# Optimization experiments

Hardware: AMD Instinct MI355X
Metric: run time of the kernel (lower is better)

## Reference

```python
import jax, jax.numpy as jnp
import numpy as np

SQRT_QKV_DIM = 8.0  # sqrt(qkv_dim=64)


def setup_inputs() -> dict:
    key = jax.random.key(0)
    ks = jax.random.split(key, 8)
    B, H, T, M, d, hid = 4, 16, 512, 512, 64, 16
    return {
        "q": jax.random.normal(ks[0], (B, H, T, d), dtype=jnp.float32),
        "k": jax.random.normal(ks[1], (B, H, M, d), dtype=jnp.float32),
        "v": jax.random.normal(ks[2], (B, H, M, d), dtype=jnp.float32),
        "D_TM": jax.random.uniform(ks[3], (B, T, M), dtype=jnp.float32),
        "mix1_weight": jax.random.uniform(ks[4], (H, 2, hid), minval=-0.7071, maxval=0.7071, dtype=jnp.float32),
        "mix1_bias": jax.random.uniform(ks[5], (H, hid), minval=-0.7071, maxval=0.7071, dtype=jnp.float32),
        "mix2_weight": jax.random.uniform(ks[6], (H, hid, 1), minval=-0.25, maxval=0.25, dtype=jnp.float32),
        "mix2_bias": jax.random.uniform(ks[7], (H, 1), minval=-0.25, maxval=0.25, dtype=jnp.float32),
    }


def reference(q, k, v, D_TM, mix1_weight, mix1_bias, mix2_weight, mix2_bias):
    B, H, T, d = q.shape
    Mc = k.shape[2]
    # scaled dot-product score: (B,H,T,M)
    dot_score = jnp.einsum("bhtd,bhmd->bhtm", q, k) / SQRT_QKV_DIM
    # per-head 2->hidden->1 MLP mixing dot score and distance bias.
    # Avoid explicit stack: linear layer over the 2 score channels expands as
    # dot*W1[:,0,:] + D*W1[:,1,:].  ms1: (B,H,T,M,hid)
    w1_dot = mix1_weight[:, 0, :][None, :, None, None, :]   # (1,H,1,1,hid)
    w1_dist = mix1_weight[:, 1, :][None, :, None, None, :]
    ms1 = (dot_score[..., None] * w1_dot
           + D_TM[:, None, :, :, None] * w1_dist
           + mix1_bias[None, :, None, None, :])
    ms1 = jax.nn.relu(ms1)
    # hidden -> 1: mixed_scores (B,H,T,M)
    mixed = jnp.einsum("bhtmc,hc->bhtm", ms1, mix2_weight[:, :, 0])
    mixed = mixed + mix2_bias[:, 0][None, :, None, None]
    weights = jax.nn.softmax(mixed, axis=3)
    out = jnp.einsum("bhtm,bhmd->bhtd", weights, v)   # (B,H,T,d)
    return out.transpose(0, 2, 1, 3).reshape(B, T, H * d)
```

## Files before the change

kernel.cpp:

```cpp
#include <hip/hip_runtime.h>
#include <stdint.h>

typedef __attribute__((ext_vector_type(8))) short short8;
typedef __attribute__((ext_vector_type(4))) float floatx4;
typedef __attribute__((ext_vector_type(2))) float float2v;

#define MFMA(a, b, c) __builtin_amdgcn_mfma_f32_16x16x32_bf16(a, b, c, 0, 0, 0)

union Frag { uint32_t u[4]; short8 s; };

__device__ __forceinline__ void packsplit(float a, float b, uint32_t& hi, uint32_t& lo) {
    uint32_t ua = __float_as_uint(a), ub = __float_as_uint(b);
    uint32_t ha = ua & 0xFFFF0000u, hb = ub & 0xFFFF0000u;
    float ra = a - __uint_as_float(ha);
    float rb = b - __uint_as_float(hb);
    hi = __builtin_amdgcn_perm(ub, ua, 0x07060302u);
    lo = __builtin_amdgcn_perm(__float_as_uint(rb), __float_as_uint(ra), 0x07060302u);
}

__device__ __forceinline__ float fexp2(float x) {
#if __has_builtin(__builtin_amdgcn_exp2f)
    return __builtin_amdgcn_exp2f(x);
#else
    return exp2f(x);
#endif
}

__device__ __forceinline__ void bar_lds() {
    asm volatile("s_waitcnt lgkmcnt(0)" ::: "memory");
    __builtin_amdgcn_s_barrier();
    __builtin_amdgcn_sched_barrier(0);
}


__global__ __launch_bounds__(512)
void msmha_flash(const float* __restrict__ qg, const float* __restrict__ kg,
                 const float* __restrict__ vg, const float* __restrict__ Dg,
                 const float* __restrict__ m1w, const float* __restrict__ m1b,
                 const float* __restrict__ m2w, const float* __restrict__ m2b,
                 float* __restrict__ outg) {
    __shared__ __align__(16) uint32_t sm[17408];
    __shared__ __align__(16) float4 wlds[16];

    const int tid   = threadIdx.x;
    const int w     = tid >> 6;
    const int group = w >> 2;
    const int gw    = w & 3;
    const int lane  = tid & 63;
    const int col   = lane & 15;
    const int quad  = lane >> 4;
    const int gtid  = tid & 255;

    const int bid = blockIdx.x;
    const int wgT = bid >> 6;
    const int bh  = bid & 63;
    const int h   = bh & 15;
    const int b   = bh >> 4;
    const int t0g = wgT * 64;

    const size_t base = (size_t)bh * 512 * 64;
    const float LOG2E = 1.4426950408889634f;

    if (tid < 16) {
        const float w1d = m1w[h * 32 + tid];
        const float w1s = m1w[h * 32 + 16 + tid];
        const float b1  = m1b[h * 16 + tid];
        const float w2  = m2w[h * 16 + tid];
        wlds[tid] = make_float4(w1d * (0.125f * LOG2E), w1s * LOG2E, b1 * LOG2E, 0.5f * w2);
    }

    const int krow = 16 * gw + (lane >> 2);
    const int kqt  = lane & 3;
    const int ksw  = (krow & 7) << 2;
    const int rsw  = (col & 7) << 2;
    const int dgrp = gtid & 15;
    const int m4   = gtid >> 4;
    const int cpV  = (2 * m4 + 8 * ((dgrp >> 1) & 3)) & 31;
    const int rsel = col >> 3;

    const int gb = group * 8704;
    uint32_t* KH = sm + gb;
    uint32_t* KL = sm + gb + 2048;
    uint32_t* VH = sm + gb + 4096;
    uint32_t* VL = sm + gb + 6400;

    const int moff = group * 256;
    const float* kc = kg + base + (size_t)moff * 64;
    const float* vc = vg + base + (size_t)moff * 64;
    const float* Dc = Dg + ((size_t)b * 512 + t0g + gw * 16 + col) * 512 + moff + quad * 4;

    float4 kp[4];
#pragma unroll
    for (int i = 0; i < 4; ++i)
        kp[i] = *(const float4*)(kc + (size_t)krow * 64 + 16 * i + 4 * kqt);

    float sA = 0.f, sB = 0.f, sC = 0.f;
#pragma unroll 1
    for (int c = 0; c < 16; ++c) {
        const float w2 = m2w[h * 16 + c];
        sA = fmaf(w2, m1w[h * 32 + c], sA);
        sB = fmaf(w2, m1w[h * 32 + 16 + c], sB);
        sC = fmaf(w2, m1b[h * 16 + c], sC);
    }
    const float Ac = sA * (0.0625f * LOG2E);
    const float Bc = sB * (0.5f * LOG2E);
    const float Cc = fmaf(0.5f, sC, m2b[h]) * LOG2E;

    Frag qh[2], ql[2];
    {
        const float* qrow = qg + base + (size_t)(t0g + gw * 16 + col) * 64;
#pragma unroll
        for (int ks = 0; ks < 2; ++ks) {
            const float4 f0 = *(const float4*)(qrow + ks * 32 + quad * 8);
            const float4 f1 = *(const float4*)(qrow + ks * 32 + quad * 8 + 4);
            packsplit(f0.x, f0.y, qh[ks].u[0], ql[ks].u[0]);
            packsplit(f0.z, f0.w, qh[ks].u[1], ql[ks].u[1]);
            packsplit(f1.x, f1.y, qh[ks].u[2], ql[ks].u[2]);
            packsplit(f1.z, f1.w, qh[ks].u[3], ql[ks].u[3]);
        }
    }

    float lsx = 0.f, lsy = 0.f;
    floatx4 oacc[4];
#pragma unroll
    for (int dt = 0; dt < 4; ++dt) oacc[dt] = floatx4{0.f, 0.f, 0.f, 0.f};

    const float2v Ac2 = {Ac, Ac}, Bc2 = {Bc, Bc}, Cc2 = {Cc, Cc};

#pragma unroll
    for (int mc = 0; mc < 4; ++mc) {
        float4 vp[4], dp[4];
#pragma unroll
        for (int i = 0; i < 4; ++i)
            vp[i] = *(const float4*)(vc + (size_t)(mc * 64 + 4 * m4 + i) * 64 + dgrp * 4);
#pragma unroll
        for (int mt = 0; mt < 4; ++mt)
            dp[mt] = *(const float4*)(Dc + mc * 64 + mt * 16);

#pragma unroll
        for (int i = 0; i < 4; ++i) {
            uint32_t h0, l0, h1, l1;
            packsplit(kp[i].x, kp[i].y, h0, l0);
            packsplit(kp[i].z, kp[i].w, h1, l1);
            const int off = (8 * i + 2 * kqt) ^ ksw;
            *(uint2*)(KH + krow * 32 + off) = make_uint2(h0, h1);
            *(uint2*)(KL + krow * 32 + off) = make_uint2(l0, l1);
        }
        if (mc < 3) {
#pragma unroll
            for (int i = 0; i < 4; ++i)
                kp[i] = *(const float4*)(kc + (size_t)((mc + 1) * 64 + krow) * 64 + 16 * i + 4 * kqt);
        }
        bar_lds();

        floatx4 sc[4];
        __builtin_amdgcn_s_setprio(1);
#pragma unroll
        for (int mt = 0; mt < 4; ++mt) {
            floatx4 acc = {0.f, 0.f, 0.f, 0.f};
#pragma unroll
            for (int ks = 0; ks < 2; ++ks) {
                const int ro = (mt * 16 + col) * 32 + ((16 * ks + 4 * quad) ^ rsw);
                Frag ah, al;
                ah.s = *(const short8*)(KH + ro);
                al.s = *(const short8*)(KL + ro);
                acc = MFMA(ah.s, qh[ks].s, acc);
                acc = MFMA(ah.s, ql[ks].s, acc);
                acc = MFMA(al.s, qh[ks].s, acc);
            }
            sc[mt] = acc;
        }
        __builtin_amdgcn_s_setprio(0);

#pragma unroll
        for (int jj = 0; jj < 4; ++jj) {
            uint32_t h0, l0, h1, l1;
            packsplit(((const float*)&vp[0])[jj], ((const float*)&vp[1])[jj], h0, l0);
            packsplit(((const float*)&vp[2])[jj], ((const float*)&vp[3])[jj], h1, l1);
            const int d = 4 * dgrp + jj;
            *(uint2*)(VH + d * 36 + cpV) = make_uint2(h0, h1);
            *(uint2*)(VL + d * 36 + cpV) = make_uint2(l0, l1);
        }

        float2v scp[8], dvp[8], mixp[8];
#pragma unroll
        for (int mt = 0; mt < 4; ++mt) {
            scp[2 * mt]     = float2v{sc[mt][0], sc[mt][1]};
            scp[2 * mt + 1] = float2v{sc[mt][2], sc[mt][3]};
            dvp[2 * mt]     = float2v{dp[mt].x, dp[mt].y};
            dvp[2 * mt + 1] = float2v{dp[mt].z, dp[mt].w};
        }
#pragma unroll
        for (int e = 0; e < 8; ++e) mixp[e] = dvp[e] * Bc2 + Cc2;
#pragma unroll 4
        for (int c = 0; c < 16; ++c) {
            const float4 wv = wlds[c];
            const float2v wx = {wv.x, wv.x}, wy = {wv.y, wv.y};
            const float2v wz = {wv.z, wv.z}, ww = {wv.w, wv.w};
#pragma unroll
            for (int e = 0; e < 8; ++e) {
                const float2v hh = scp[e] * wx + (dvp[e] * wy + wz);
                const float2v ah = __builtin_elementwise_max(hh, -hh);
                mixp[e] = ah * ww + mixp[e];
            }
        }
#pragma unroll
        for (int e = 0; e < 8; ++e) {
            const float2v s2 = scp[e] * Ac2 + mixp[e];
            const float px = fexp2(s2.x);
            const float py = fexp2(s2.y);
            scp[e] = float2v{px, py};
            lsx += px; lsy += py;
        }

        bar_lds();

        const int prow = (gw * 16 + col) * 32;
#pragma unroll
        for (int mt = 0; mt < 4; ++mt) {
            uint32_t h0, l0, h1, l1;
            packsplit(scp[2 * mt].x, scp[2 * mt].y, h0, l0);
            packsplit(scp[2 * mt + 1].x, scp[2 * mt + 1].y, h1, l1);
            const int off = (mt * 8 + 2 * quad) ^ rsw;
            *(uint2*)(KH + prow + off) = make_uint2(h0, h1);
            *(uint2*)(KL + prow + off) = make_uint2(l0, l1);
        }

        __builtin_amdgcn_s_setprio(1);
#pragma unroll
        for (int ks = 0; ks < 2; ++ks) {
            const int po = prow + ((16 * ks + 4 * quad) ^ rsw);
            Frag pah, pal;
            pah.s = *(const short8*)(KH + po);
            pal.s = *(const short8*)(KL + po);
#pragma unroll
            for (int dt = 0; dt < 4; ++dt) {
                const int cbd = ((16 * ks + 4 * quad) + 8 * ((2 * dt + rsel) & 3)) & 31;
                const int vo = (dt * 16 + col) * 36 + cbd;
                Frag bhv, blv;
                bhv.s = *(const short8*)(VH + vo);
                blv.s = *(const short8*)(VL + vo);
                oacc[dt] = MFMA(pah.s, bhv.s, oacc[dt]);
                oacc[dt] = MFMA(pah.s, blv.s, oacc[dt]);
                oacc[dt] = MFMA(pal.s, bhv.s, oacc[dt]);
            }
        }
        __builtin_amdgcn_s_setprio(0);
    }

    bar_lds();

    float lsum = lsx + lsy;
    lsum += __shfl_xor(lsum, 16, 64);
    lsum += __shfl_xor(lsum, 32, 64);

    float* smf = (float*)sm;
    if (group == 1) {
        if (quad == 0) smf[12864 + gw * 16 + col] = lsum;
        const int t = gw * 16 + quad * 4;
#pragma unroll
        for (int dt = 0; dt < 4; ++dt)
#pragma unroll
            for (int r = 0; r < 4; ++r)
                smf[8704 + (t + r) * 65 + dt * 16 + col] = oacc[dt][r];
    }
    bar_lds();
    if (group == 0) {
        const float l1c = smf[12864 + gw * 16 + col];
        const float rdn = 1.f / (lsum + l1c);
        float rdT[4];
#pragma unroll
        for (int r = 0; r < 4; ++r)
            rdT[r] = __shfl(rdn, quad * 4 + r, 64);
        const int t = gw * 16 + quad * 4;
        const size_t obase = ((size_t)b * 512 + t0g + t) * 1024 + h * 64 + col;
#pragma unroll
        for (int dt = 0; dt < 4; ++dt)
#pragma unroll
            for (int r = 0; r < 4; ++r) {
                const float o1 = smf[8704 + (t + r) * 65 + dt * 16 + col];
                outg[obase + (size_t)r * 1024 + dt * 16] = (oacc[dt][r] + o1) * rdT[r];
            }
    }
}

extern "C" void kernel_launch(void* const* d_in, const int* in_sizes, int n_in,
                              void* d_out, int out_size, void* d_ws, size_t ws_size,
                              hipStream_t stream) {
    const float* q   = (const float*)d_in[0];
    const float* k   = (const float*)d_in[1];
    const float* v   = (const float*)d_in[2];
    const float* dtm = (const float*)d_in[3];
    const float* m1w = (const float*)d_in[4];
    const float* m1b = (const float*)d_in[5];
    const float* m2w = (const float*)d_in[6];
    const float* m2b = (const float*)d_in[7];
    float* out = (float*)d_out;

    dim3 grid(4 * 16 * 8);
    dim3 block(512);
    msmha_flash<<<grid, block, 0, stream>>>(q, k, v, dtm, m1w, m1b, m2w, m2b, out);
}
```

Measured before the change: 131.0 us.

## Cut register pressure: scalar mixing MLP, no K prefetch, waves_per_eu hint

Replaces the packed float2 mixing-MLP math with scalar fmaf/fabs computed in two halves, which shrinks live register arrays. Drops the cross-iteration K prefetch so K is loaded at the start of each chunk, and stops unrolling the chunk loop. Adds an amdgpu_waves_per_eu(4) hint. The aim is lower VGPR usage so more waves fit per EU, at the cost of losing packed-FMA throughput and exposing K load latency.

Result: faster. 123.9 us (-5.4%).

```diff
diff --git a/kernel.cpp b/kernel.cpp
--- a/kernel.cpp
+++ b/kernel.cpp
@@ -3,7 +3,6 @@
 
 typedef __attribute__((ext_vector_type(8))) short short8;
 typedef __attribute__((ext_vector_type(4))) float floatx4;
-typedef __attribute__((ext_vector_type(2))) float float2v;
 
 #define MFMA(a, b, c) __builtin_amdgcn_mfma_f32_16x16x32_bf16(a, b, c, 0, 0, 0)
 
@@ -33,6 +32,7 @@
 }
 
 
+__attribute__((amdgpu_waves_per_eu(4)))
 __global__ __launch_bounds__(512)
 void msmha_flash(const float* __restrict__ qg, const float* __restrict__ kg,
                  const float* __restrict__ vg, const float* __restrict__ Dg,
@@ -89,11 +89,6 @@
     const float* vc = vg + base + (size_t)moff * 64;
     const float* Dc = Dg + ((size_t)b * 512 + t0g + gw * 16 + col) * 512 + moff + quad * 4;
 
-    float4 kp[4];
-#pragma unroll
-    for (int i = 0; i < 4; ++i)
-        kp[i] = *(const float4*)(kc + (size_t)krow * 64 + 16 * i + 4 * kqt);
-
     float sA = 0.f, sB = 0.f, sC = 0.f;
 #pragma unroll 1
     for (int c = 0; c < 16; ++c) {
@@ -120,16 +115,17 @@
         }
     }
 
-    float lsx = 0.f, lsy = 0.f;
+    float lsum = 0.f;
     floatx4 oacc[4];
 #pragma unroll
     for (int dt = 0; dt < 4; ++dt) oacc[dt] = floatx4{0.f, 0.f, 0.f, 0.f};
 
-    const float2v Ac2 = {Ac, Ac}, Bc2 = {Bc, Bc}, Cc2 = {Cc, Cc};
-
-#pragma unroll
+#pragma unroll 1
     for (int mc = 0; mc < 4; ++mc) {
-        float4 vp[4], dp[4];
+        float4 kp[4], vp[4], dp[4];
+#pragma unroll
+        for (int i = 0; i < 4; ++i)
+            kp[i] = *(const float4*)(kc + (size_t)(mc * 64 + krow) * 64 + 16 * i + 4 * kqt);
 #pragma unroll
         for (int i = 0; i < 4; ++i)
             vp[i] = *(const float4*)(vc + (size_t)(mc * 64 + 4 * m4 + i) * 64 + dgrp * 4);
@@ -145,11 +141,6 @@
             const int off = (8 * i + 2 * kqt) ^ ksw;
             *(uint2*)(KH + krow * 32 + off) = make_uint2(h0, h1);
             *(uint2*)(KL + krow * 32 + off) = make_uint2(l0, l1);
-        }
-        if (mc < 3) {
-#pragma unroll
-            for (int i = 0; i < 4; ++i)
-                kp[i] = *(const float4*)(kc + (size_t)((mc + 1) * 64 + krow) * 64 + 16 * i + 4 * kqt);
         }
         bar_lds();
 
@@ -182,35 +173,34 @@
             *(uint2*)(VL + d * 36 + cpV) = make_uint2(l0, l1);
         }
 
-        float2v scp[8], dvp[8], mixp[8];
-#pragma unroll
-        for (int mt = 0; mt < 4; ++mt) {
-            scp[2 * mt]     = float2v{sc[mt][0], sc[mt][1]};
-            scp[2 * mt + 1] = float2v{sc[mt][2], sc[mt][3]};
-            dvp[2 * mt]     = float2v{dp[mt].x, dp[mt].y};
-            dvp[2 * mt + 1] = float2v{dp[mt].z, dp[mt].w};
-        }
-#pragma unroll
-        for (int e = 0; e < 8; ++e) mixp[e] = dvp[e] * Bc2 + Cc2;
+#pragma unroll
+        for (int half = 0; half < 2; ++half) {
+            float dvf[8], mix[8];
+#pragma unroll
+            for (int q2 = 0; q2 < 2; ++q2) {
+                const float4 dd = dp[2 * half + q2];
+                dvf[q2 * 4 + 0] = dd.x; dvf[q2 * 4 + 1] = dd.y;
+                dvf[q2 * 4 + 2] = dd.z; dvf[q2 * 4 + 3] = dd.w;
+            }
+#pragma unroll
+            for (int e = 0; e < 8; ++e) mix[e] = fmaf(dvf[e], Bc, Cc);
 #pragma unroll 4
-        for (int c = 0; c < 16; ++c) {
-            const float4 wv = wlds[c];
-            const float2v wx = {wv.x, wv.x}, wy = {wv.y, wv.y};
-            const float2v wz = {wv.z, wv.z}, ww = {wv.w, wv.w};
+            for (int c = 0; c < 16; ++c) {
+                const float4 wv = wlds[c];
+#pragma unroll
+                for (int e = 0; e < 8; ++e) {
+                    const float s = sc[2 * half + (e >> 2)][e & 3];
+                    const float hh = fmaf(s, wv.x, fmaf(dvf[e], wv.y, wv.z));
+                    mix[e] = fmaf(fabsf(hh), wv.w, mix[e]);
+                }
+            }
 #pragma unroll
             for (int e = 0; e < 8; ++e) {
-                const float2v hh = scp[e] * wx + (dvp[e] * wy + wz);
-                const float2v ah = __builtin_elementwise_max(hh, -hh);
-                mixp[e] = ah * ww + mixp[e];
-            }
-        }
-#pragma unroll
-        for (int e = 0; e < 8; ++e) {
-            const float2v s2 = scp[e] * Ac2 + mixp[e];
-            const float px = fexp2(s2.x);
-            const float py = fexp2(s2.y);
-            scp[e] = float2v{px, py};
-            lsx += px; lsy += py;
+                const float s = sc[2 * half + (e >> 2)][e & 3];
+                const float p = fexp2(fmaf(s, Ac, mix[e]));
+                sc[2 * half + (e >> 2)][e & 3] = p;
+                lsum += p;
+            }
         }
 
         bar_lds();
@@ -219,8 +209,8 @@
 #pragma unroll
         for (int mt = 0; mt < 4; ++mt) {
             uint32_t h0, l0, h1, l1;
-            packsplit(scp[2 * mt].x, scp[2 * mt].y, h0, l0);
-            packsplit(scp[2 * mt + 1].x, scp[2 * mt + 1].y, h1, l1);
+            packsplit(sc[mt][0], sc[mt][1], h0, l0);
+            packsplit(sc[mt][2], sc[mt][3], h1, l1);
             const int off = (mt * 8 + 2 * quad) ^ rsw;
             *(uint2*)(KH + prow + off) = make_uint2(h0, h1);
             *(uint2*)(KL + prow + off) = make_uint2(l0, l1);
@@ -250,7 +240,6 @@
 
     bar_lds();
 
-    float lsum = lsx + lsy;
     lsum += __shfl_xor(lsum, 16, 64);
     lsum += __shfl_xor(lsum, 32, 64);
 
```
